# Kernel tuning notes

Measured on AMD Instinct MI355X. Metric: run time of the kernel, lower is better.

## Reference

```python
import jax, jax.numpy as jnp
import numpy as np
from jax.scipy.special import logsumexp

EPSILON = 0.1
N_ITERS = 5


def setup_inputs() -> dict:
    key = jax.random.key(0)
    k1, k2, k3 = jax.random.split(key, 3)
    B, Q, T, D = 16, 1024, 1024, 256
    preds = jax.random.normal(k1, (B, Q, D), dtype=jnp.float32)
    targets = jax.random.normal(k2, (B, T, D), dtype=jnp.float32)
    filter = jax.random.normal(k3, (B, T), dtype=jnp.float32)
    return {"preds": preds, "targets": targets, "filter": filter}


def _cdist(x, y):
    x2 = jnp.sum(x * x, axis=-1)[:, :, None]          # [B,Q,1]
    y2 = jnp.sum(y * y, axis=-1)[:, None, :]          # [B,1,T]
    xy = jnp.einsum("bqd,btd->bqt", x, y)             # [B,Q,T]
    return jnp.sqrt(jnp.maximum(x2 + y2 - 2.0 * xy, 0.0))


def reference(preds, targets, filter):
    eps = EPSILON
    B, Q, _ = preds.shape
    T = targets.shape[1]
    cost = _cdist(preds, targets)                     # [B,Q,T]
    filter_cost = 2.0 * jnp.max(cost)
    cost = jnp.where(filter[:, None, :] <= 0, filter_cost, cost)
    u = jnp.zeros((B, Q), dtype=cost.dtype)
    v = jnp.zeros((B, T), dtype=cost.dtype)
    for _ in range(N_ITERS):
        u = -eps * logsumexp(-(cost - v[:, None, :]) / eps, axis=2)
        v = -eps * logsumexp(-(cost - u[:, :, None]) / eps, axis=1)
    P = jnp.exp((u[:, :, None] + v[:, None, :] - cost) / eps)
    idx_tgt = jnp.argmax(P, axis=2)
    return (idx_tgt, P)
```

## Files before the change

kernel.cpp:

```cpp
#include <hip/hip_runtime.h>
#include <math.h>

#define BB 16
#define QQ 1024
#define TT 1024
#define DD 256
#define EPS 0.1f
#define SINK_ITERS 5
#define FCONST 128.0f
#define K2 14.426950408889634f
#define EPSLN2 0.069314718055994531f

typedef _Float16 f16;
typedef _Float16 f16x4 __attribute__((ext_vector_type(4)));
typedef _Float16 f16x8 __attribute__((ext_vector_type(8)));
typedef float f32x4 __attribute__((ext_vector_type(4)));

__device__ __forceinline__ float fast_exp2(float x) {
#if __has_builtin(__builtin_amdgcn_exp2f)
  return __builtin_amdgcn_exp2f(x);
#else
  return exp2f(x);
#endif
}
__device__ __forceinline__ float fast_log2(float x) {
#if __has_builtin(__builtin_amdgcn_logf)
  return __builtin_amdgcn_logf(x);
#else
  return log2f(x);
#endif
}

__global__ __launch_bounds__(256) void cvt_kernel(
    const float* __restrict__ preds, const float* __restrict__ targets,
    f16* __restrict__ Ahi, f16* __restrict__ Alo,
    f16* __restrict__ Bhi, f16* __restrict__ Blo,
    float* __restrict__ x2, float* __restrict__ y2)
{
  int w = threadIdx.x >> 6, l = threadIdx.x & 63;
  int row = blockIdx.x * 4 + w;
  const float* src; f16 *hi, *lo; float* nrm;
  if (row < BB*QQ) {
    src = preds + (size_t)row * DD;
    hi = Ahi + (size_t)row * DD; lo = Alo + (size_t)row * DD; nrm = x2 + row;
  } else {
    int r = row - BB*QQ;
    src = targets + (size_t)r * DD;
    hi = Bhi + (size_t)r * DD; lo = Blo + (size_t)r * DD; nrm = y2 + r;
  }
  float4 v = ((const float4*)src)[l];
  f16x4 h, lw;
  h.x = (f16)v.x; h.y = (f16)v.y; h.z = (f16)v.z; h.w = (f16)v.w;
  lw.x = (f16)(v.x - (float)h.x); lw.y = (f16)(v.y - (float)h.y);
  lw.z = (f16)(v.z - (float)h.z); lw.w = (f16)(v.w - (float)h.w);
  *(f16x4*)(hi + l*4) = h;
  *(f16x4*)(lo + l*4) = lw;
  float s = v.x*v.x + v.y*v.y + v.z*v.z + v.w*v.w;
  #pragma unroll
  for (int o = 32; o; o >>= 1) s += __shfl_down(s, o, 64);
  if (l == 0) *nrm = s;
}

__global__ __launch_bounds__(256) void cost_mfma_kernel(
    const f16* __restrict__ Ahi, const f16* __restrict__ Alo,
    const f16* __restrict__ Bhi, const f16* __restrict__ Blo,
    const float* __restrict__ x2, const float* __restrict__ y2,
    const float* __restrict__ filter,
    float* __restrict__ cost, float* __restrict__ costT, int useT)
{
  __shared__ f16 sA[2][128*32];
  __shared__ f16 sB[2][128*32];
  int b = blockIdx.z;
  int q0 = blockIdx.y * 128, t0 = blockIdx.x * 128;
  int tid = threadIdx.x, w = tid >> 6, l = tid & 63;
  int rq = (w >> 1) * 64, rt = (w & 1) * 64;
  int fr = l & 15, fg = l >> 4;
  const f16* pA[2] = { Ahi + ((size_t)b*QQ + q0) * DD, Alo + ((size_t)b*QQ + q0) * DD };
  const f16* pB[2] = { Bhi + ((size_t)b*TT + t0) * DD, Blo + ((size_t)b*TT + t0) * DD };
  f32x4 acc[4][4] = {};
  for (int k0 = 0; k0 < DD; k0 += 32) {
    __syncthreads();
#if __has_builtin(__builtin_amdgcn_global_load_lds)
    #pragma unroll
    for (int j = 0; j < 2; ++j) {
      int chunk = w*128 + j*64 + l;
      int row = chunk >> 2, kc = chunk & 3;
      size_t go = (size_t)row * DD + k0 + kc*8;
      int lb = (w*128 + j*64) * 8;
      #pragma unroll
      for (int h = 0; h < 2; ++h) {
        __builtin_amdgcn_global_load_lds(
            (const __attribute__((address_space(1))) void*)(pA[h] + go),
            (__attribute__((address_space(3))) void*)&sA[h][lb], 16, 0, 0);
        __builtin_amdgcn_global_load_lds(
            (const __attribute__((address_space(1))) void*)(pB[h] + go),
            (__attribute__((address_space(3))) void*)&sB[h][lb], 16, 0, 0);
      }
    }
#else
    #pragma unroll
    for (int j = 0; j < 2; ++j) {
      int chunk = w*128 + j*64 + l;
      int row = chunk >> 2, kc = chunk & 3;
      size_t go = (size_t)row * DD + k0 + kc*8;
      #pragma unroll
      for (int h = 0; h < 2; ++h) {
        *(f16x8*)&sA[h][chunk*8] = *(const f16x8*)(pA[h] + go);
        *(f16x8*)&sB[h][chunk*8] = *(const f16x8*)(pB[h] + go);
      }
    }
#endif
    __syncthreads();
    f16x8 ah[4], al[4], bh[4], bl[4];
    #pragma unroll
    for (int f = 0; f < 4; ++f) {
      int ao = (rq + f*16 + fr)*32 + fg*8;
      ah[f] = *(const f16x8*)&sA[0][ao];
      al[f] = *(const f16x8*)&sA[1][ao];
      int bo = (rt + f*16 + fr)*32 + fg*8;
      bh[f] = *(const f16x8*)&sB[0][bo];
      bl[f] = *(const f16x8*)&sB[1][bo];
    }
    #pragma unroll
    for (int fm = 0; fm < 4; ++fm)
      #pragma unroll
      for (int fn = 0; fn < 4; ++fn) {
        acc[fm][fn] = __builtin_amdgcn_mfma_f32_16x16x32_f16(ah[fm], bh[fn], acc[fm][fn], 0, 0, 0);
        acc[fm][fn] = __builtin_amdgcn_mfma_f32_16x16x32_f16(ah[fm], bl[fn], acc[fm][fn], 0, 0, 0);
        acc[fm][fn] = __builtin_amdgcn_mfma_f32_16x16x32_f16(al[fm], bh[fn], acc[fm][fn], 0, 0, 0);
      }
  }
  float xv[16];
  #pragma unroll
  for (int fm = 0; fm < 4; ++fm)
    #pragma unroll
    for (int r = 0; r < 4; ++r)
      xv[fm*4+r] = x2[(size_t)b*QQ + q0 + rq + fm*16 + fg*4 + r];
  float yv[4], fv[4];
  #pragma unroll
  for (int fn = 0; fn < 4; ++fn) {
    int t = t0 + rt + fn*16 + fr;
    yv[fn] = y2[(size_t)b*TT + t];
    fv[fn] = filter[(size_t)b*TT + t];
  }
  #pragma unroll
  for (int fm = 0; fm < 4; ++fm) {
    #pragma unroll
    for (int fn = 0; fn < 4; ++fn) {
      int t = t0 + rt + fn*16 + fr;
      float cvr[4];
      #pragma unroll
      for (int r = 0; r < 4; ++r) {
        float c2 = xv[fm*4+r] + yv[fn] - 2.0f*acc[fm][fn][r];
        float c = sqrtf(fmaxf(c2, 0.f));
        if (fv[fn] <= 0.f) c = FCONST;
        cvr[r] = c;
        int q = q0 + rq + fm*16 + fg*4 + r;
        cost[((size_t)b*QQ + q)*TT + t] = c;
      }
      if (useT && fv[fn] > 0.f) {
        float* dst = costT + ((size_t)b*TT + t)*QQ + q0 + rq + fm*16 + fg*4;
        *(float4*)dst = make_float4(cvr[0], cvr[1], cvr[2], cvr[3]);
      }
    }
  }
}

__global__ __launch_bounds__(64) void norms_kernel(
    const float* __restrict__ preds, const float* __restrict__ targets,
    float* __restrict__ x2, float* __restrict__ y2)
{
  int row = blockIdx.x;
  const float* src; float* dst;
  if (row < BB*QQ) { src = preds + (size_t)row * DD; dst = x2 + row; }
  else { int r = row - BB*QQ; src = targets + (size_t)r * DD; dst = y2 + r; }
  float4 v = ((const float4*)src)[threadIdx.x];
  float s = v.x*v.x + v.y*v.y + v.z*v.z + v.w*v.w;
  #pragma unroll
  for (int o = 32; o; o >>= 1) s += __shfl_down(s, o, 64);
  if (threadIdx.x == 0) *dst = s;
}

#define LDSTR 132
__global__ __launch_bounds__(256) void cost_fp32_kernel(
    const float* __restrict__ preds, const float* __restrict__ targets,
    const float* __restrict__ x2, const float* __restrict__ y2,
    const float* __restrict__ filter,
    float* __restrict__ cost, float* __restrict__ costT, int useT)
{
  __shared__ float As[16*LDSTR];
  __shared__ float Bs[16*LDSTR];
  int b  = blockIdx.z;
  int q0 = blockIdx.y * 128;
  int t0 = blockIdx.x * 128;
  const float* Ab = preds   + ((size_t)b*QQ + q0) * DD;
  const float* Bb = targets + ((size_t)b*TT + t0) * DD;
  int tid = threadIdx.x;
  int srow = tid >> 2, sq = (tid & 3) << 2;
  int w = tid >> 6, l = tid & 63;
  int rq = ((w >> 1) << 6) + ((l >> 3) << 3);
  int rt = ((w & 1) << 6) + ((l & 7) << 3);
  float acc[8][8] = {};
  for (int k0 = 0; k0 < DD; k0 += 16) {
    float4 a0 = *(const float4*)(Ab + (size_t)srow*DD + k0 + sq);
    float4 a1 = *(const float4*)(Ab + (size_t)(srow+64)*DD + k0 + sq);
    float4 b0 = *(const float4*)(Bb + (size_t)srow*DD + k0 + sq);
    float4 b1 = *(const float4*)(Bb + (size_t)(srow+64)*DD + k0 + sq);
    __syncthreads();
    As[(sq+0)*LDSTR + srow] = a0.x; As[(sq+1)*LDSTR + srow] = a0.y;
    As[(sq+2)*LDSTR + srow] = a0.z; As[(sq+3)*LDSTR + srow] = a0.w;
    As[(sq+0)*LDSTR + srow+64] = a1.x; As[(sq+1)*LDSTR + srow+64] = a1.y;
    As[(sq+2)*LDSTR + srow+64] = a1.z; As[(sq+3)*LDSTR + srow+64] = a1.w;
    Bs[(sq+0)*LDSTR + srow] = b0.x; Bs[(sq+1)*LDSTR + srow] = b0.y;
    Bs[(sq+2)*LDSTR + srow] = b0.z; Bs[(sq+3)*LDSTR + srow] = b0.w;
    Bs[(sq+0)*LDSTR + srow+64] = b1.x; Bs[(sq+1)*LDSTR + srow+64] = b1.y;
    Bs[(sq+2)*LDSTR + srow+64] = b1.z; Bs[(sq+3)*LDSTR + srow+64] = b1.w;
    __syncthreads();
    #pragma unroll
    for (int k = 0; k < 16; ++k) {
      float4 af0 = *(const float4*)&As[k*LDSTR + rq];
      float4 af1 = *(const float4*)&As[k*LDSTR + rq + 4];
      float4 bf0 = *(const float4*)&Bs[k*LDSTR + rt];
      float4 bf1 = *(const float4*)&Bs[k*LDSTR + rt + 4];
      float aa[8] = {af0.x,af0.y,af0.z,af0.w,af1.x,af1.y,af1.z,af1.w};
      float bb[8] = {bf0.x,bf0.y,bf0.z,bf0.w,bf1.x,bf1.y,bf1.z,bf1.w};
      #pragma unroll
      for (int i = 0; i < 8; ++i)
        #pragma unroll
        for (int j = 0; j < 8; ++j)
          acc[i][j] = fmaf(aa[i], bb[j], acc[i][j]);
    }
  }
  float xq[8], yt[8], fvv[8];
  #pragma unroll
  for (int i = 0; i < 8; ++i) xq[i] = x2[(size_t)b*QQ + q0 + rq + i];
  #pragma unroll
  for (int j = 0; j < 8; ++j) {
    yt[j] = y2[(size_t)b*TT + t0 + rt + j];
    fvv[j] = filter[(size_t)b*TT + t0 + rt + j];
  }
  float cv[8][8];
  #pragma unroll
  for (int i = 0; i < 8; ++i)
    #pragma unroll
    for (int j = 0; j < 8; ++j) {
      float c2 = xq[i] + yt[j] - 2.f*acc[i][j];
      float c = sqrtf(fmaxf(c2, 0.f));
      if (fvv[j] <= 0.f) c = FCONST;
      cv[i][j] = c;
    }
  #pragma unroll
  for (int i = 0; i < 8; ++i) {
    float* dst = cost + ((size_t)b*QQ + q0 + rq + i) * TT + t0 + rt;
    *(float4*)dst       = make_float4(cv[i][0], cv[i][1], cv[i][2], cv[i][3]);
    *(float4*)(dst + 4) = make_float4(cv[i][4], cv[i][5], cv[i][6], cv[i][7]);
  }
  if (useT) {
    #pragma unroll
    for (int j = 0; j < 8; ++j) {
      if (fvv[j] <= 0.f) continue;
      float* dst = costT + ((size_t)b*TT + t0 + rt + j) * QQ + q0 + rq;
      *(float4*)dst       = make_float4(cv[0][j], cv[1][j], cv[2][j], cv[3][j]);
      *(float4*)(dst + 4) = make_float4(cv[4][j], cv[5][j], cv[6][j], cv[7][j]);
    }
  }
}

__device__ __forceinline__ float wave_max64(float v) {
  #pragma unroll
  for (int o = 1; o < 64; o <<= 1) v = fmaxf(v, __shfl_xor(v, o, 64));
  return v;
}
__device__ __forceinline__ float wave_sum64(float v) {
  #pragma unroll
  for (int o = 1; o < 64; o <<= 1) v += __shfl_xor(v, o, 64);
  return v;
}

__global__ __launch_bounds__(256) void u_kernel(
    const float* __restrict__ cost, const float* __restrict__ v, float* __restrict__ u)
{
  int w = threadIdx.x >> 6, l = threadIdx.x & 63;
  int row = blockIdx.x * 8 + w * 2;
  int b = row >> 10;
  const float4* c0 = (const float4*)(cost + (size_t)row * TT);
  const float4* c1 = c0 + TT/4;
  const float4* vb = (const float4*)(v + (size_t)b * TT);
  float s0[16], s1[16], m0 = -3.0e38f, m1 = -3.0e38f;
  #pragma unroll
  for (int i = 0; i < 4; ++i) {
    float4 v4 = vb[l + (i << 6)];
    float4 a4 = c0[l + (i << 6)];
    float4 b4 = c1[l + (i << 6)];
    s0[4*i+0] = (v4.x - a4.x) * K2; s0[4*i+1] = (v4.y - a4.y) * K2;
    s0[4*i+2] = (v4.z - a4.z) * K2; s0[4*i+3] = (v4.w - a4.w) * K2;
    s1[4*i+0] = (v4.x - b4.x) * K2; s1[4*i+1] = (v4.y - b4.y) * K2;
    s1[4*i+2] = (v4.z - b4.z) * K2; s1[4*i+3] = (v4.w - b4.w) * K2;
    m0 = fmaxf(m0, fmaxf(fmaxf(s0[4*i+0], s0[4*i+1]), fmaxf(s0[4*i+2], s0[4*i+3])));
    m1 = fmaxf(m1, fmaxf(fmaxf(s1[4*i+0], s1[4*i+1]), fmaxf(s1[4*i+2], s1[4*i+3])));
  }
  m0 = wave_max64(m0); m1 = wave_max64(m1);
  float q0 = 0.f, q1 = 0.f;
  #pragma unroll
  for (int i = 0; i < 16; ++i) { q0 += fast_exp2(s0[i] - m0); q1 += fast_exp2(s1[i] - m1); }
  q0 = wave_sum64(q0); q1 = wave_sum64(q1);
  if (l == 0) {
    u[row]   = -EPSLN2 * (m0 + fast_log2(q0));
    u[row+1] = -EPSLN2 * (m1 + fast_log2(q1));
  }
}

__global__ __launch_bounds__(256) void v_kernel(
    const float* __restrict__ cost, const float* __restrict__ costT, int useT,
    const float* __restrict__ filter, const float* __restrict__ u, float* __restrict__ v)
{
  int w = threadIdx.x >> 6, l = threadIdx.x & 63;
  int row = blockIdx.x * 8 + w * 2;
  int b = row >> 10, t = row & 1023;
  const float4* ub = (const float4*)(u + (size_t)b * QQ);
  bool f0 = (filter[row]   <= 0.f);
  bool f1 = (filter[row+1] <= 0.f);
  float4 uw[4];
  #pragma unroll
  for (int i = 0; i < 4; ++i) uw[i] = ub[l + (i << 6)];
  float s0[16], s1[16], m0 = -3.0e38f, m1 = -3.0e38f;
  if (f0) {
    #pragma unroll
    for (int i = 0; i < 4; ++i) {
      s0[4*i+0] = (uw[i].x - FCONST) * K2; s0[4*i+1] = (uw[i].y - FCONST) * K2;
      s0[4*i+2] = (uw[i].z - FCONST) * K2; s0[4*i+3] = (uw[i].w - FCONST) * K2;
    }
  } else if (useT) {
    const float4* cr = (const float4*)(costT + (size_t)row * QQ);
    #pragma unroll
    for (int i = 0; i < 4; ++i) {
      float4 c4 = cr[l + (i << 6)];
      s0[4*i+0] = (uw[i].x - c4.x) * K2; s0[4*i+1] = (uw[i].y - c4.y) * K2;
      s0[4*i+2] = (uw[i].z - c4.z) * K2; s0[4*i+3] = (uw[i].w - c4.w) * K2;
    }
  } else {
    const float* cr = cost + (size_t)b*QQ*TT + t;
    #pragma unroll
    for (int i = 0; i < 4; ++i) {
      int q = (l + (i << 6)) << 2;
      s0[4*i+0] = (uw[i].x - cr[(size_t)(q+0)*TT]) * K2;
      s0[4*i+1] = (uw[i].y - cr[(size_t)(q+1)*TT]) * K2;
      s0[4*i+2] = (uw[i].z - cr[(size_t)(q+2)*TT]) * K2;
      s0[4*i+3] = (uw[i].w - cr[(size_t)(q+3)*TT]) * K2;
    }
  }
  if (f1) {
    #pragma unroll
    for (int i = 0; i < 4; ++i) {
      s1[4*i+0] = (uw[i].x - FCONST) * K2; s1[4*i+1] = (uw[i].y - FCONST) * K2;
      s1[4*i+2] = (uw[i].z - FCONST) * K2; s1[4*i+3] = (uw[i].w - FCONST) * K2;
    }
  } else if (useT) {
    const float4* cr = (const float4*)(costT + (size_t)(row+1) * QQ);
    #pragma unroll
    for (int i = 0; i < 4; ++i) {
      float4 c4 = cr[l + (i << 6)];
      s1[4*i+0] = (uw[i].x - c4.x) * K2; s1[4*i+1] = (uw[i].y - c4.y) * K2;
      s1[4*i+2] = (uw[i].z - c4.z) * K2; s1[4*i+3] = (uw[i].w - c4.w) * K2;
    }
  } else {
    const float* cr = cost + (size_t)b*QQ*TT + t + 1;
    #pragma unroll
    for (int i = 0; i < 4; ++i) {
      int q = (l + (i << 6)) << 2;
      s1[4*i+0] = (uw[i].x - cr[(size_t)(q+0)*TT]) * K2;
      s1[4*i+1] = (uw[i].y - cr[(size_t)(q+1)*TT]) * K2;
      s1[4*i+2] = (uw[i].z - cr[(size_t)(q+2)*TT]) * K2;
      s1[4*i+3] = (uw[i].w - cr[(size_t)(q+3)*TT]) * K2;
    }
  }
  #pragma unroll
  for (int i = 0; i < 16; ++i) { m0 = fmaxf(m0, s0[i]); m1 = fmaxf(m1, s1[i]); }
  m0 = wave_max64(m0); m1 = wave_max64(m1);
  float q0 = 0.f, q1 = 0.f;
  #pragma unroll
  for (int i = 0; i < 16; ++i) { q0 += fast_exp2(s0[i] - m0); q1 += fast_exp2(s1[i] - m1); }
  q0 = wave_sum64(q0); q1 = wave_sum64(q1);
  if (l == 0) {
    v[row]   = -EPSLN2 * (m0 + fast_log2(q0));
    v[row+1] = -EPSLN2 * (m1 + fast_log2(q1));
  }
}

__global__ __launch_bounds__(256) void p_kernel(
    float* __restrict__ P, const float* __restrict__ u, const float* __restrict__ v,
    float* __restrict__ idxOut)
{
  int w = threadIdx.x >> 6, l = threadIdx.x & 63;
  int row = blockIdx.x * 8 + w * 2;
  int b = row >> 10;
  float4* c0 = (float4*)(P + (size_t)row * TT);
  float4* c1 = c0 + TT/4;
  const float4* vb = (const float4*)(v + (size_t)b * TT);
  float u0 = u[row], u1 = u[row+1];
  float bp0 = -1.f, bp1 = -1.f; int bt0 = 0, bt1 = 0;
  #pragma unroll
  for (int i = 0; i < 4; ++i) {
    float4 v4 = vb[l + (i << 6)];
    float4 a4 = c0[l + (i << 6)];
    float4 b4 = c1[l + (i << 6)];
    int t0 = (l + (i << 6)) << 2;
    float4 p0, p1;
    p0.x = fast_exp2((u0 + v4.x - a4.x) * K2);
    p0.y = fast_exp2((u0 + v4.y - a4.y) * K2);
    p0.z = fast_exp2((u0 + v4.z - a4.z) * K2);
    p0.w = fast_exp2((u0 + v4.w - a4.w) * K2);
    p1.x = fast_exp2((u1 + v4.x - b4.x) * K2);
    p1.y = fast_exp2((u1 + v4.y - b4.y) * K2);
    p1.z = fast_exp2((u1 + v4.z - b4.z) * K2);
    p1.w = fast_exp2((u1 + v4.w - b4.w) * K2);
    if (p0.x > bp0) { bp0 = p0.x; bt0 = t0 + 0; }
    if (p0.y > bp0) { bp0 = p0.y; bt0 = t0 + 1; }
    if (p0.z > bp0) { bp0 = p0.z; bt0 = t0 + 2; }
    if (p0.w > bp0) { bp0 = p0.w; bt0 = t0 + 3; }
    if (p1.x > bp1) { bp1 = p1.x; bt1 = t0 + 0; }
    if (p1.y > bp1) { bp1 = p1.y; bt1 = t0 + 1; }
    if (p1.z > bp1) { bp1 = p1.z; bt1 = t0 + 2; }
    if (p1.w > bp1) { bp1 = p1.w; bt1 = t0 + 3; }
    c0[l + (i << 6)] = p0;
    c1[l + (i << 6)] = p1;
  }
  #pragma unroll
  for (int o = 1; o < 64; o <<= 1) {
    float op = __shfl_xor(bp0, o, 64);
    int   ot = __shfl_xor(bt0, o, 64);
    if (op > bp0 || (op == bp0 && ot < bt0)) { bp0 = op; bt0 = ot; }
    op = __shfl_xor(bp1, o, 64);
    ot = __shfl_xor(bt1, o, 64);
    if (op > bp1 || (op == bp1 && ot < bt1)) { bp1 = op; bt1 = ot; }
  }
  if (l == 0) { idxOut[row] = (float)bt0; idxOut[row+1] = (float)bt1; }
}

extern "C" void kernel_launch(void* const* d_in, const int* in_sizes, int n_in,
                              void* d_out, int out_size, void* d_ws, size_t ws_size,
                              hipStream_t stream) {
  const float* preds   = (const float*)d_in[0];
  const float* targets = (const float*)d_in[1];
  const float* filter  = (const float*)d_in[2];
  float* out = (float*)d_out;
  float* idxOut = out;
  float* P = out + (size_t)BB*QQ;

  const size_t F16A  = (size_t)BB*QQ*DD;
  const size_t f16tot = 4 * F16A * sizeof(f16);
  const size_t smallb = (size_t)4 * 16384 * sizeof(float);
  const size_t costTB = (size_t)BB * QQ * TT * sizeof(float);

  char* p = (char*)d_ws;
  int useF16 = ws_size >= f16tot + smallb;
  f16 *Ahi, *Alo, *Bhi, *Blo;
  float *x2, *y2, *u, *v, *costT;
  int useT;
  if (useF16) {
    Ahi = (f16*)p; Alo = Ahi + F16A; Bhi = Alo + F16A; Blo = Bhi + F16A;
    x2 = (float*)(p + f16tot); y2 = x2 + 16384; u = y2 + 16384; v = u + 16384;
    useT = ws_size >= f16tot + smallb + costTB;
    costT = (float*)(p + f16tot + smallb);
  } else {
    Ahi = Alo = Bhi = Blo = nullptr;
    x2 = (float*)p; y2 = x2 + 16384; u = y2 + 16384; v = u + 16384;
    useT = ws_size >= smallb + costTB;
    costT = (float*)(p + smallb);
  }

  hipMemsetAsync(u, 0, (size_t)2 * 16384 * sizeof(float), stream);

  dim3 cg(TT/128, QQ/128, BB);
  if (useF16) {
    cvt_kernel<<<BB*(QQ+TT)/4, 256, 0, stream>>>(preds, targets, Ahi, Alo, Bhi, Blo, x2, y2);
    cost_mfma_kernel<<<cg, 256, 0, stream>>>(Ahi, Alo, Bhi, Blo, x2, y2, filter, P, costT, useT);
  } else {
    norms_kernel<<<BB*(QQ+TT), 64, 0, stream>>>(preds, targets, x2, y2);
    cost_fp32_kernel<<<cg, 256, 0, stream>>>(preds, targets, x2, y2, filter, P, costT, useT);
  }
  int blks = BB*QQ/8;
  for (int it = 0; it < SINK_ITERS; ++it) {
    u_kernel<<<blks, 256, 0, stream>>>(P, v, u);
    v_kernel<<<blks, 256, 0, stream>>>(P, costT, useT, filter, u, v);
  }
  p_kernel<<<blks, 256, 0, stream>>>(P, u, v, idxOut);
}
```

Before: 263.6 us.

## Fuse Sinkhorn iterations and final pass into one cooperative persistent kernel

```diff
diff --git a/kernel.cpp b/kernel.cpp
--- a/kernel.cpp
+++ b/kernel.cpp
@@ -1,5 +1,8 @@
 #include <hip/hip_runtime.h>
+#include <hip/hip_cooperative_groups.h>
 #include <math.h>
+
+namespace cg = cooperative_groups;
 
 #define BB 16
 #define QQ 1024
@@ -277,11 +280,9 @@
   return v;
 }
 
-__global__ __launch_bounds__(256) void u_kernel(
+__device__ __forceinline__ void u_body(int row, int l, bool it0,
     const float* __restrict__ cost, const float* __restrict__ v, float* __restrict__ u)
 {
-  int w = threadIdx.x >> 6, l = threadIdx.x & 63;
-  int row = blockIdx.x * 8 + w * 2;
   int b = row >> 10;
   const float4* c0 = (const float4*)(cost + (size_t)row * TT);
   const float4* c1 = c0 + TT/4;
@@ -289,7 +290,9 @@
   float s0[16], s1[16], m0 = -3.0e38f, m1 = -3.0e38f;
   #pragma unroll
   for (int i = 0; i < 4; ++i) {
-    float4 v4 = vb[l + (i << 6)];
+    float4 v4;
+    if (it0) v4 = make_float4(0.f, 0.f, 0.f, 0.f);
+    else     v4 = vb[l + (i << 6)];
     float4 a4 = c0[l + (i << 6)];
     float4 b4 = c1[l + (i << 6)];
     s0[4*i+0] = (v4.x - a4.x) * K2; s0[4*i+1] = (v4.y - a4.y) * K2;
@@ -310,12 +313,10 @@
   }
 }
 
-__global__ __launch_bounds__(256) void v_kernel(
+__device__ __forceinline__ void v_body(int row, int l,
     const float* __restrict__ cost, const float* __restrict__ costT, int useT,
     const float* __restrict__ filter, const float* __restrict__ u, float* __restrict__ v)
 {
-  int w = threadIdx.x >> 6, l = threadIdx.x & 63;
-  int row = blockIdx.x * 8 + w * 2;
   int b = row >> 10, t = row & 1023;
   const float4* ub = (const float4*)(u + (size_t)b * QQ);
   bool f0 = (filter[row]   <= 0.f);
@@ -387,12 +388,10 @@
   }
 }
 
-__global__ __launch_bounds__(256) void p_kernel(
+__device__ __forceinline__ void p_body(int row, int l,
     float* __restrict__ P, const float* __restrict__ u, const float* __restrict__ v,
     float* __restrict__ idxOut)
 {
-  int w = threadIdx.x >> 6, l = threadIdx.x & 63;
-  int row = blockIdx.x * 8 + w * 2;
   int b = row >> 10;
   float4* c0 = (float4*)(P + (size_t)row * TT);
   float4* c1 = c0 + TT/4;
@@ -437,6 +436,44 @@
   if (l == 0) { idxOut[row] = (float)bt0; idxOut[row+1] = (float)bt1; }
 }
 
+__global__ __launch_bounds__(256, 4) void sweep_kernel(
+    float* __restrict__ P, const float* __restrict__ costT, int useT,
+    const float* __restrict__ filter, float* __restrict__ u, float* __restrict__ v,
+    float* __restrict__ idxOut, int G)
+{
+  cg::grid_group grid = cg::this_grid();
+  const int w = threadIdx.x >> 6, l = threadIdx.x & 63;
+  for (int it = 0; it < SINK_ITERS; ++it) {
+    const bool it0 = (it == 0);
+    for (int row = blockIdx.x*8 + w*2; row < BB*QQ; row += G*8)
+      u_body(row, l, it0, P, v, u);
+    grid.sync();
+    for (int row = blockIdx.x*8 + w*2; row < BB*TT; row += G*8)
+      v_body(row, l, P, costT, useT, filter, u, v);
+    grid.sync();
+  }
+  for (int row = blockIdx.x*8 + w*2; row < BB*QQ; row += G*8)
+    p_body(row, l, P, u, v, idxOut);
+}
+
+__global__ __launch_bounds__(256) void u_kernel(
+    const float* __restrict__ cost, const float* __restrict__ v, float* __restrict__ u, int it0)
+{
+  u_body(blockIdx.x * 8 + (threadIdx.x >> 6) * 2, threadIdx.x & 63, it0 != 0, cost, v, u);
+}
+__global__ __launch_bounds__(256) void v_kernel(
+    const float* __restrict__ cost, const float* __restrict__ costT, int useT,
+    const float* __restrict__ filter, const float* __restrict__ u, float* __restrict__ v)
+{
+  v_body(blockIdx.x * 8 + (threadIdx.x >> 6) * 2, threadIdx.x & 63, cost, costT, useT, filter, u, v);
+}
+__global__ __launch_bounds__(256) void p_kernel(
+    float* __restrict__ P, const float* __restrict__ u, const float* __restrict__ v,
+    float* __restrict__ idxOut)
+{
+  p_body(blockIdx.x * 8 + (threadIdx.x >> 6) * 2, threadIdx.x & 63, P, u, v, idxOut);
+}
+
 extern "C" void kernel_launch(void* const* d_in, const int* in_sizes, int n_in,
                               void* d_out, int out_size, void* d_ws, size_t ws_size,
                               hipStream_t stream) {
@@ -469,20 +506,37 @@
     costT = (float*)(p + smallb);
   }
 
-  hipMemsetAsync(u, 0, (size_t)2 * 16384 * sizeof(float), stream);
-
-  dim3 cg(TT/128, QQ/128, BB);
+  dim3 cg_(TT/128, QQ/128, BB);
   if (useF16) {
     cvt_kernel<<<BB*(QQ+TT)/4, 256, 0, stream>>>(preds, targets, Ahi, Alo, Bhi, Blo, x2, y2);
-    cost_mfma_kernel<<<cg, 256, 0, stream>>>(Ahi, Alo, Bhi, Blo, x2, y2, filter, P, costT, useT);
+    cost_mfma_kernel<<<cg_, 256, 0, stream>>>(Ahi, Alo, Bhi, Blo, x2, y2, filter, P, costT, useT);
   } else {
     norms_kernel<<<BB*(QQ+TT), 64, 0, stream>>>(preds, targets, x2, y2);
-    cost_fp32_kernel<<<cg, 256, 0, stream>>>(preds, targets, x2, y2, filter, P, costT, useT);
-  }
-  int blks = BB*QQ/8;
-  for (int it = 0; it < SINK_ITERS; ++it) {
-    u_kernel<<<blks, 256, 0, stream>>>(P, v, u);
-    v_kernel<<<blks, 256, 0, stream>>>(P, costT, useT, filter, u, v);
-  }
-  p_kernel<<<blks, 256, 0, stream>>>(P, u, v, idxOut);
-}
+    cost_fp32_kernel<<<cg_, 256, 0, stream>>>(preds, targets, x2, y2, filter, P, costT, useT);
+  }
+
+  int coop = 0, dev = 0;
+  (void)hipGetDevice(&dev);
+  (void)hipDeviceGetAttribute(&coop, hipDeviceAttributeCooperativeLaunch, dev);
+  if (coop) {
+    int G = 1024;
+    int ncu = 0;
+    if (hipDeviceGetAttribute(&ncu, hipDeviceAttributeMultiprocessorCount, dev) == hipSuccess && ncu > 0) {
+      int nb = 0;
+      if (hipOccupancyMaxActiveBlocksPerMultiprocessor(&nb, (const void*)sweep_kernel, 256, 0) == hipSuccess && nb > 0) {
+        G = nb * ncu;
+        if (G > 1024) G = 1024;
+      }
+    }
+    void* args[] = { (void*)&P, (void*)&costT, (void*)&useT, (void*)&filter,
+                     (void*)&u, (void*)&v, (void*)&idxOut, (void*)&G };
+    (void)hipLaunchCooperativeKernel((const void*)sweep_kernel, dim3(G), dim3(256), args, 0, stream);
+  } else {
+    int blks = BB*QQ/8;
+    for (int it = 0; it < SINK_ITERS; ++it) {
+      u_kernel<<<blks, 256, 0, stream>>>(P, v, u, it == 0 ? 1 : 0);
+      v_kernel<<<blks, 256, 0, stream>>>(P, costT, useT, filter, u, v);
+    }
+    p_kernel<<<blks, 256, 0, stream>>>(P, u, v, idxOut);
+  }
+}
```

Result: slower. 832.1 us (+215.6%).

## Compact cost columns by filter mask to skip filtered targets in Sinkhorn

Applied to the files above, without the earlier changes.

```diff
diff --git a/kernel.cpp b/kernel.cpp
--- a/kernel.cpp
+++ b/kernel.cpp
@@ -61,12 +61,49 @@
   if (l == 0) *nrm = s;
 }
 
+__global__ __launch_bounds__(256) void scan_kernel(
+    const float* __restrict__ filter, int* __restrict__ nU,
+    int* __restrict__ f0i, int* __restrict__ cidx)
+{
+  __shared__ int sc[256];
+  __shared__ int sf0;
+  int b = blockIdx.x, tid = threadIdx.x;
+  if (tid == 0) sf0 = 0x7fffffff;
+  __syncthreads();
+  float4 f4 = ((const float4*)(filter + (size_t)b*TT))[tid];
+  int i0 = f4.x > 0.f, i1 = f4.y > 0.f, i2 = f4.z > 0.f, i3 = f4.w > 0.f;
+  int cnt = i0+i1+i2+i3;
+  int t0 = tid*4;
+  int lf = 0x7fffffff;
+  if (!i0) lf = t0; else if (!i1) lf = t0+1; else if (!i2) lf = t0+2; else if (!i3) lf = t0+3;
+  if (lf != 0x7fffffff) atomicMin(&sf0, lf);
+  sc[tid] = cnt;
+  __syncthreads();
+  for (int off = 1; off < 256; off <<= 1) {
+    int val = (tid >= off) ? sc[tid-off] : 0;
+    __syncthreads();
+    sc[tid] += val;
+    __syncthreads();
+  }
+  int excl = sc[tid] - cnt;
+  int* cb = cidx + (size_t)b*TT + t0;
+  int run = excl;
+  cb[0] = run; run += i0;
+  cb[1] = run; run += i1;
+  cb[2] = run; run += i2;
+  cb[3] = run; run += i3;
+  if (tid == 255) nU[b] = sc[255];
+  __syncthreads();
+  if (tid == 0) f0i[b] = sf0;
+}
+
 __global__ __launch_bounds__(256) void cost_mfma_kernel(
     const f16* __restrict__ Ahi, const f16* __restrict__ Alo,
     const f16* __restrict__ Bhi, const f16* __restrict__ Blo,
     const float* __restrict__ x2, const float* __restrict__ y2,
     const float* __restrict__ filter,
-    float* __restrict__ cost, float* __restrict__ costT, int useT)
+    float* __restrict__ cost, float* __restrict__ costT, int useT,
+    float* __restrict__ costC, const int* __restrict__ cidx, int compact)
 {
   __shared__ f16 sA[2][128*32];
   __shared__ f16 sB[2][128*32];
@@ -137,11 +174,13 @@
     for (int r = 0; r < 4; ++r)
       xv[fm*4+r] = x2[(size_t)b*QQ + q0 + rq + fm*16 + fg*4 + r];
   float yv[4], fv[4];
+  int jn[4];
   #pragma unroll
   for (int fn = 0; fn < 4; ++fn) {
     int t = t0 + rt + fn*16 + fr;
     yv[fn] = y2[(size_t)b*TT + t];
     fv[fn] = filter[(size_t)b*TT + t];
+    jn[fn] = compact ? cidx[(size_t)b*TT + t] : 0;
   }
   #pragma unroll
   for (int fm = 0; fm < 4; ++fm) {
@@ -152,11 +191,14 @@
       #pragma unroll
       for (int r = 0; r < 4; ++r) {
         float c2 = xv[fm*4+r] + yv[fn] - 2.0f*acc[fm][fn][r];
-        float c = sqrtf(fmaxf(c2, 0.f));
-        if (fv[fn] <= 0.f) c = FCONST;
-        cvr[r] = c;
+        float craw = sqrtf(fmaxf(c2, 0.f));
+        cvr[r] = craw;
         int q = q0 + rq + fm*16 + fg*4 + r;
-        cost[((size_t)b*QQ + q)*TT + t] = c;
+        if (!compact) {
+          cost[((size_t)b*QQ + q)*TT + t] = (fv[fn] <= 0.f) ? FCONST : craw;
+        } else if (fv[fn] > 0.f) {
+          costC[((size_t)b*QQ + q)*TT + jn[fn]] = craw;
+        }
       }
       if (useT && fv[fn] > 0.f) {
         float* dst = costT + ((size_t)b*TT + t)*QQ + q0 + rq + fm*16 + fg*4;
@@ -277,11 +319,200 @@
   return v;
 }
 
-__global__ __launch_bounds__(256) void u_kernel(
-    const float* __restrict__ cost, const float* __restrict__ v, float* __restrict__ u)
+__global__ __launch_bounds__(256) void u_c_kernel(
+    const float* __restrict__ costC, const float* __restrict__ vC,
+    const float* __restrict__ vf, const int* __restrict__ nU,
+    float* __restrict__ u, int it0)
 {
   int w = threadIdx.x >> 6, l = threadIdx.x & 63;
   int row = blockIdx.x * 8 + w * 2;
+  int b = row >> 10;
+  int n = nU[b];
+  int nF = TT - n;
+  const float4* c0 = (const float4*)(costC + (size_t)row * TT);
+  const float4* c1 = c0 + TT/4;
+  const float4* vb = (const float4*)(vC + (size_t)b * TT);
+  float s0[16], s1[16], m0 = -3.0e38f, m1 = -3.0e38f;
+  int iters = (n + 255) >> 8;
+  #pragma unroll
+  for (int i = 0; i < 4; ++i) {
+    if (i < iters) {
+      int jj = l + (i << 6);
+      int j = jj << 2;
+      float4 v4;
+      if (it0) v4 = make_float4(0.f,0.f,0.f,0.f); else v4 = vb[jj];
+      float4 a4 = c0[jj];
+      float4 b4 = c1[jj];
+      s0[4*i+0] = (j+0 < n) ? (v4.x - a4.x)*K2 : -3.0e38f;
+      s0[4*i+1] = (j+1 < n) ? (v4.y - a4.y)*K2 : -3.0e38f;
+      s0[4*i+2] = (j+2 < n) ? (v4.z - a4.z)*K2 : -3.0e38f;
+      s0[4*i+3] = (j+3 < n) ? (v4.w - a4.w)*K2 : -3.0e38f;
+      s1[4*i+0] = (j+0 < n) ? (v4.x - b4.x)*K2 : -3.0e38f;
+      s1[4*i+1] = (j+1 < n) ? (v4.y - b4.y)*K2 : -3.0e38f;
+      s1[4*i+2] = (j+2 < n) ? (v4.z - b4.z)*K2 : -3.0e38f;
+      s1[4*i+3] = (j+3 < n) ? (v4.w - b4.w)*K2 : -3.0e38f;
+      m0 = fmaxf(m0, fmaxf(fmaxf(s0[4*i+0], s0[4*i+1]), fmaxf(s0[4*i+2], s0[4*i+3])));
+      m1 = fmaxf(m1, fmaxf(fmaxf(s1[4*i+0], s1[4*i+1]), fmaxf(s1[4*i+2], s1[4*i+3])));
+    } else {
+      #pragma unroll
+      for (int k = 0; k < 4; ++k) { s0[4*i+k] = -3.0e38f; s1[4*i+k] = -3.0e38f; }
+    }
+  }
+  float st = 0.f;
+  if (nF > 0) {
+    float vfb = it0 ? 0.f : vf[b];
+    st = (vfb - FCONST) * K2;
+    m0 = fmaxf(m0, st); m1 = fmaxf(m1, st);
+  }
+  m0 = wave_max64(m0); m1 = wave_max64(m1);
+  float q0 = 0.f, q1 = 0.f;
+  #pragma unroll
+  for (int i = 0; i < 16; ++i) { q0 += fast_exp2(s0[i] - m0); q1 += fast_exp2(s1[i] - m1); }
+  q0 = wave_sum64(q0); q1 = wave_sum64(q1);
+  if (nF > 0) {
+    q0 += (float)nF * fast_exp2(st - m0);
+    q1 += (float)nF * fast_exp2(st - m1);
+  }
+  if (l == 0) {
+    u[row]   = -EPSLN2 * (m0 + fast_log2(q0));
+    u[row+1] = -EPSLN2 * (m1 + fast_log2(q1));
+  }
+}
+
+__global__ __launch_bounds__(256) void v_c_kernel(
+    const float* __restrict__ costT,
+    const float* __restrict__ filter, const int* __restrict__ cidx,
+    const float* __restrict__ u, float* __restrict__ v,
+    float* __restrict__ vC, float* __restrict__ vf)
+{
+  int w = threadIdx.x >> 6, l = threadIdx.x & 63;
+  int row = blockIdx.x * 8 + w * 2;
+  int b = row >> 10;
+  const float4* ub = (const float4*)(u + (size_t)b * QQ);
+  bool f0 = (filter[row]   <= 0.f);
+  bool f1 = (filter[row+1] <= 0.f);
+  float4 uw[4];
+  #pragma unroll
+  for (int i = 0; i < 4; ++i) uw[i] = ub[l + (i << 6)];
+  float s0[16], s1[16], m0 = -3.0e38f, m1 = -3.0e38f;
+  if (f0) {
+    #pragma unroll
+    for (int i = 0; i < 4; ++i) {
+      s0[4*i+0] = (uw[i].x - FCONST) * K2; s0[4*i+1] = (uw[i].y - FCONST) * K2;
+      s0[4*i+2] = (uw[i].z - FCONST) * K2; s0[4*i+3] = (uw[i].w - FCONST) * K2;
+    }
+  } else {
+    const float4* cr = (const float4*)(costT + (size_t)row * QQ);
+    #pragma unroll
+    for (int i = 0; i < 4; ++i) {
+      float4 c4 = cr[l + (i << 6)];
+      s0[4*i+0] = (uw[i].x - c4.x) * K2; s0[4*i+1] = (uw[i].y - c4.y) * K2;
+      s0[4*i+2] = (uw[i].z - c4.z) * K2; s0[4*i+3] = (uw[i].w - c4.w) * K2;
+    }
+  }
+  if (f1) {
+    #pragma unroll
+    for (int i = 0; i < 4; ++i) {
+      s1[4*i+0] = (uw[i].x - FCONST) * K2; s1[4*i+1] = (uw[i].y - FCONST) * K2;
+      s1[4*i+2] = (uw[i].z - FCONST) * K2; s1[4*i+3] = (uw[i].w - FCONST) * K2;
+    }
+  } else {
+    const float4* cr = (const float4*)(costT + (size_t)(row+1) * QQ);
+    #pragma unroll
+    for (int i = 0; i < 4; ++i) {
+      float4 c4 = cr[l + (i << 6)];
+      s1[4*i+0] = (uw[i].x - c4.x) * K2; s1[4*i+1] = (uw[i].y - c4.y) * K2;
+      s1[4*i+2] = (uw[i].z - c4.z) * K2; s1[4*i+3] = (uw[i].w - c4.w) * K2;
+    }
+  }
+  #pragma unroll
+  for (int i = 0; i < 16; ++i) { m0 = fmaxf(m0, s0[i]); m1 = fmaxf(m1, s1[i]); }
+  m0 = wave_max64(m0); m1 = wave_max64(m1);
+  float q0 = 0.f, q1 = 0.f;
+  #pragma unroll
+  for (int i = 0; i < 16; ++i) { q0 += fast_exp2(s0[i] - m0); q1 += fast_exp2(s1[i] - m1); }
+  q0 = wave_sum64(q0); q1 = wave_sum64(q1);
+  if (l == 0) {
+    float val0 = -EPSLN2 * (m0 + fast_log2(q0));
+    float val1 = -EPSLN2 * (m1 + fast_log2(q1));
+    v[row]   = val0;
+    v[row+1] = val1;
+    if (f0) vf[b] = val0; else vC[(size_t)b*TT + cidx[row]] = val0;
+    if (f1) vf[b] = val1; else vC[(size_t)b*TT + cidx[row+1]] = val1;
+  }
+}
+
+__global__ __launch_bounds__(256) void p_c_kernel(
+    const float* __restrict__ costC, const float* __restrict__ filter,
+    const int* __restrict__ cidx, const int* __restrict__ nU,
+    const int* __restrict__ f0i, const float* __restrict__ vf,
+    const float* __restrict__ u, const float* __restrict__ v,
+    float* __restrict__ P, float* __restrict__ idxOut)
+{
+  int w = threadIdx.x >> 6, l = threadIdx.x & 63;
+  int row = blockIdx.x * 8 + w * 2;
+  int b = row >> 10;
+  int nF = TT - nU[b];
+  float u0 = u[row], u1 = u[row+1];
+  float pf0 = -1.f, pf1 = -1.f; int fidx = 0x7fffffff;
+  if (nF > 0) {
+    float vfb = vf[b];
+    pf0 = fast_exp2((u0 + vfb - FCONST) * K2);
+    pf1 = fast_exp2((u1 + vfb - FCONST) * K2);
+    fidx = f0i[b];
+  }
+  const float* r0 = costC + (size_t)row * TT;
+  const float* r1 = r0 + TT;
+  float4* o0 = (float4*)(P + (size_t)row * TT);
+  float4* o1 = o0 + TT/4;
+  const float4* fb = (const float4*)(filter + (size_t)b * TT);
+  const int4*   jb = (const int4*)(cidx + (size_t)b * TT);
+  const float4* vv = (const float4*)(v + (size_t)b * TT);
+  float bp0 = -1.f, bp1 = -1.f; int bt0 = 0x7ffffffe, bt1 = 0x7ffffffe;
+  #pragma unroll
+  for (int i = 0; i < 4; ++i) {
+    int e = l + (i << 6);
+    float4 f4 = fb[e];
+    int4  j4 = jb[e];
+    float4 v4 = vv[e];
+    int tb = e << 2;
+    float4 p0, p1;
+#define PELEM(comp, jx, toff) \
+    if (f4.comp > 0.f) { \
+      float cA = r0[jx], cB = r1[jx]; \
+      p0.comp = fast_exp2((u0 + v4.comp - cA) * K2); \
+      p1.comp = fast_exp2((u1 + v4.comp - cB) * K2); \
+      if (p0.comp > bp0) { bp0 = p0.comp; bt0 = tb + toff; } \
+      if (p1.comp > bp1) { bp1 = p1.comp; bt1 = tb + toff; } \
+    } else { p0.comp = pf0; p1.comp = pf1; }
+    PELEM(x, j4.x, 0)
+    PELEM(y, j4.y, 1)
+    PELEM(z, j4.z, 2)
+    PELEM(w, j4.w, 3)
+#undef PELEM
+    o0[e] = p0;
+    o1[e] = p1;
+  }
+  #pragma unroll
+  for (int o = 1; o < 64; o <<= 1) {
+    float op = __shfl_xor(bp0, o, 64);
+    int   ot = __shfl_xor(bt0, o, 64);
+    if (op > bp0 || (op == bp0 && ot < bt0)) { bp0 = op; bt0 = ot; }
+    op = __shfl_xor(bp1, o, 64);
+    ot = __shfl_xor(bt1, o, 64);
+    if (op > bp1 || (op == bp1 && ot < bt1)) { bp1 = op; bt1 = ot; }
+  }
+  if (l == 0) {
+    if (pf0 > bp0 || (pf0 == bp0 && fidx < bt0)) bt0 = fidx;
+    if (pf1 > bp1 || (pf1 == bp1 && fidx < bt1)) bt1 = fidx;
+    idxOut[row]   = (float)bt0;
+    idxOut[row+1] = (float)bt1;
+  }
+}
+
+__device__ __forceinline__ void u_body(int row, int l, bool it0,
+    const float* __restrict__ cost, const float* __restrict__ v, float* __restrict__ u)
+{
   int b = row >> 10;
   const float4* c0 = (const float4*)(cost + (size_t)row * TT);
   const float4* c1 = c0 + TT/4;
@@ -289,7 +520,9 @@
   float s0[16], s1[16], m0 = -3.0e38f, m1 = -3.0e38f;
   #pragma unroll
   for (int i = 0; i < 4; ++i) {
-    float4 v4 = vb[l + (i << 6)];
+    float4 v4;
+    if (it0) v4 = make_float4(0.f, 0.f, 0.f, 0.f);
+    else     v4 = vb[l + (i << 6)];
     float4 a4 = c0[l + (i << 6)];
     float4 b4 = c1[l + (i << 6)];
     s0[4*i+0] = (v4.x - a4.x) * K2; s0[4*i+1] = (v4.y - a4.y) * K2;
@@ -308,6 +541,12 @@
     u[row]   = -EPSLN2 * (m0 + fast_log2(q0));
     u[row+1] = -EPSLN2 * (m1 + fast_log2(q1));
   }
+}
+
+__global__ __launch_bounds__(256) void u_kernel(
+    const float* __restrict__ cost, const float* __restrict__ v, float* __restrict__ u, int it0)
+{
+  u_body(blockIdx.x * 8 + (threadIdx.x >> 6) * 2, threadIdx.x & 63, it0 != 0, cost, v, u);
 }
 
 __global__ __launch_bounds__(256) void v_kernel(
@@ -447,42 +686,52 @@
   float* idxOut = out;
   float* P = out + (size_t)BB*QQ;
 
-  const size_t F16A  = (size_t)BB*QQ*DD;
+  const size_t F16A   = (size_t)BB*QQ*DD;
   const size_t f16tot = 4 * F16A * sizeof(f16);
-  const size_t smallb = (size_t)4 * 16384 * sizeof(float);
-  const size_t costTB = (size_t)BB * QQ * TT * sizeof(float);
-
-  char* p = (char*)d_ws;
-  int useF16 = ws_size >= f16tot + smallb;
-  f16 *Ahi, *Alo, *Bhi, *Blo;
-  float *x2, *y2, *u, *v, *costT;
-  int useT;
-  if (useF16) {
-    Ahi = (f16*)p; Alo = Ahi + F16A; Bhi = Alo + F16A; Blo = Bhi + F16A;
-    x2 = (float*)(p + f16tot); y2 = x2 + 16384; u = y2 + 16384; v = u + 16384;
-    useT = ws_size >= f16tot + smallb + costTB;
-    costT = (float*)(p + f16tot + smallb);
-  } else {
-    Ahi = Alo = Bhi = Blo = nullptr;
-    x2 = (float*)p; y2 = x2 + 16384; u = y2 + 16384; v = u + 16384;
-    useT = ws_size >= smallb + costTB;
-    costT = (float*)(p + smallb);
-  }
-
-  hipMemsetAsync(u, 0, (size_t)2 * 16384 * sizeof(float), stream);
-
-  dim3 cg(TT/128, QQ/128, BB);
+  const size_t SMALL  = (size_t)1 << 19;
+  const size_t CB     = (size_t)BB * QQ * TT * sizeof(float);
+
+  char* ws = (char*)d_ws;
+  int useF16 = ws_size >= f16tot + SMALL;
+  char* base = ws + (useF16 ? f16tot : 0);
+  f16 *Ahi = (f16*)ws, *Alo = Ahi + F16A, *Bhi = Alo + F16A, *Blo = Bhi + F16A;
+  float* x2 = (float*)base;
+  float* y2 = x2 + 16384;
+  float* u  = y2 + 16384;
+  float* v  = u + 16384;
+  float* vC = v + 16384;
+  float* vf = vC + 16384;
+  int* nU   = (int*)(vf + 64);
+  int* f0i  = nU + 64;
+  int* cidx = f0i + 64;
+  float* costT = (float*)(base + SMALL);
+  float* costC = (float*)(base + SMALL + CB);
+  int useT = ws_size >= (size_t)(base - ws) + SMALL + CB;
+  int useC = useF16 && (ws_size >= f16tot + SMALL + 2*CB);
+
+  dim3 cg_(TT/128, QQ/128, BB);
   if (useF16) {
     cvt_kernel<<<BB*(QQ+TT)/4, 256, 0, stream>>>(preds, targets, Ahi, Alo, Bhi, Blo, x2, y2);
-    cost_mfma_kernel<<<cg, 256, 0, stream>>>(Ahi, Alo, Bhi, Blo, x2, y2, filter, P, costT, useT);
+    if (useC) scan_kernel<<<BB, 256, 0, stream>>>(filter, nU, f0i, cidx);
+    cost_mfma_kernel<<<cg_, 256, 0, stream>>>(Ahi, Alo, Bhi, Blo, x2, y2, filter,
+                                              P, costT, useT, costC, cidx, useC);
   } else {
     norms_kernel<<<BB*(QQ+TT), 64, 0, stream>>>(preds, targets, x2, y2);
-    cost_fp32_kernel<<<cg, 256, 0, stream>>>(preds, targets, x2, y2, filter, P, costT, useT);
-  }
+    cost_fp32_kernel<<<cg_, 256, 0, stream>>>(preds, targets, x2, y2, filter, P, costT, useT);
+  }
+
   int blks = BB*QQ/8;
-  for (int it = 0; it < SINK_ITERS; ++it) {
-    u_kernel<<<blks, 256, 0, stream>>>(P, v, u);
-    v_kernel<<<blks, 256, 0, stream>>>(P, costT, useT, filter, u, v);
-  }
-  p_kernel<<<blks, 256, 0, stream>>>(P, u, v, idxOut);
-}
+  if (useC) {
+    for (int it = 0; it < SINK_ITERS; ++it) {
+      u_c_kernel<<<blks, 256, 0, stream>>>(costC, vC, vf, nU, u, it == 0 ? 1 : 0);
+      v_c_kernel<<<blks, 256, 0, stream>>>(costT, filter, cidx, u, v, vC, vf);
+    }
+    p_c_kernel<<<blks, 256, 0, stream>>>(costC, filter, cidx, nU, f0i, vf, u, v, P, idxOut);
+  } else {
+    for (int it = 0; it < SINK_ITERS; ++it) {
+      u_kernel<<<blks, 256, 0, stream>>>(P, v, u, it == 0 ? 1 : 0);
+      v_kernel<<<blks, 256, 0, stream>>>(P, costT, useT, filter, u, v);
+    }
+    p_kernel<<<blks, 256, 0, stream>>>(P, u, v, idxOut);
+  }
+}
```

Result: no change. 267.9 us (+1.6%).
